# Performance work log

Measured on AMD Instinct MI355X. Metric: run time of the kernel, lower is better.

Reference implementation:

```python
import jax, jax.numpy as jnp
import numpy as np

EPS = 1e-5      # BatchNorm1d default eps
K = 4           # branching factor of the ontology tree
HID = 6         # num_hiddens_genotype
LEVEL_SIZES = (64, 16, 4, 1)   # leaves -> root (term_layer_list order)
OFFSETS = (0, 64, 80, 84)      # slices into the stacked [85,...] term params


def setup_inputs() -> dict:
    key = jax.random.key(0)
    ks = jax.random.split(key, 8)
    B, G, GD, NT, NL = 4096, 4096, 24, 85, 64
    f32 = jnp.float32
    return {
        "x": jax.random.normal(ks[0], (B, G), f32),
        "gene_W": jax.random.normal(ks[1], (NL, GD, G), f32) * (1.0 / np.sqrt(G)),
        "gene_b": jnp.zeros((NL, GD), f32),
        "term_W": jax.random.normal(ks[2], (NT, HID, GD), f32) * (1.0 / np.sqrt(GD)),
        "term_b": jnp.zeros((NT, HID), f32),
        "bn_gamma": jnp.ones((NT, HID), f32),
        "bn_beta": jnp.zeros((NT, HID), f32),
        "aux1_W": jax.random.normal(ks[3], (NT, 1, HID), f32) * 0.1,
        "aux1_b": jnp.zeros((NT, 1), f32),
        "aux2_W": jax.random.normal(ks[4], (NT, 1, 1), f32) * 0.1,
        "aux2_b": jnp.zeros((NT, 1), f32),
        "final_W": jax.random.normal(ks[5], (HID, HID), f32) * (1.0 / np.sqrt(HID)),
        "final_b": jnp.zeros((HID,), f32),
        "fbn_gamma": jnp.ones((HID,), f32),
        "fbn_beta": jnp.zeros((HID,), f32),
        "faux_W": jax.random.normal(ks[6], (1, HID), f32) * 0.1,
        "faux_b": jnp.zeros((1,), f32),
        "fout_W": jax.random.normal(ks[7], (1, 1), f32) * 0.1,
        "fout_b": jnp.zeros((1,), f32),
    }


def _bn(z, g, b):
    # training-mode BatchNorm1d: batch mean / biased variance over axis 0
    mu = jnp.mean(z, axis=0, keepdims=True)
    var = jnp.mean((z - mu) ** 2, axis=0, keepdims=True)
    return (z - mu) * jax.lax.rsqrt(var + EPS) * g + b


def _forward(x, gene_W, gene_b, term_W, term_b, bn_gamma, bn_beta,
             aux1_W, aux1_b, aux2_W, aux2_b, final_W, final_b,
             fbn_gamma, fbn_beta, faux_W, faux_b, fout_W, fout_b):
    B = x.shape[0]
    # direct_gene_layers for all 64 leaf terms, batched: [B, 64, 24]
    h_in = jnp.einsum('bg,tkg->btk', x, gene_W) + gene_b
    aux_outs = []
    h = None
    for n, o in zip(LEVEL_SIZES, OFFSETS):  # leaves -> root (DAG topo order)
        if h is not None:
            # concat the K=4 children hidden states of each term: [B,n,K*HID]
            h_in = h.reshape(B, n, K * HID)
        # per-term Linear + tanh + BatchNorm, batched over the n terms
        z = jnp.tanh(jnp.einsum('bti,thi->bth', h_in, term_W[o:o + n]) + term_b[o:o + n])
        h = _bn(z, bn_gamma[o:o + n], bn_beta[o:o + n])  # [B, n, HID]
        # aux head: Linear(HID->1) -> tanh -> Linear(1->1)
        a1 = jnp.tanh(jnp.einsum('bth,toh->bto', h, aux1_W[o:o + n]) + aux1_b[o:o + n])
        a2 = a1 * aux2_W[o:o + n, 0] + aux2_b[o:o + n]   # [B, n, 1]
        aux_outs.append(a2[..., 0])
    root = h[:, 0, :]                                    # [B, HID]
    f = jnp.tanh(root @ final_W.T + final_b)
    mu = jnp.mean(f, axis=0)
    var = jnp.mean((f - mu) ** 2, axis=0)
    f = (f - mu) * jax.lax.rsqrt(var + EPS) * fbn_gamma + fbn_beta
    fa = jnp.tanh(f @ faux_W.T + faux_b)                 # [B, 1]
    pred = jax.nn.sigmoid(fa * fout_W[0, 0] + fout_b)    # [B, 1]
    # aux_out_map flattened in topo order, with 'final' prediction last: [B, 86]
    return jnp.concatenate(aux_outs + [pred], axis=1)


def reference(x, gene_W, gene_b, term_W, term_b, bn_gamma, bn_beta,
              aux1_W, aux1_b, aux2_W, aux2_b, final_W, final_b,
              fbn_gamma, fbn_beta, faux_W, faux_b, fout_W, fout_b):
    return _forward(x, gene_W, gene_b, term_W, term_b, bn_gamma, bn_beta,
                    aux1_W, aux1_b, aux2_W, aux2_b, final_W, final_b,
                    fbn_gamma, fbn_beta, faux_W, faux_b, fout_W, fout_b)
```

## Files before the change

kernel.cpp:

```cpp
#include <hip/hip_runtime.h>
#include <stdint.h>
#include <math.h>

#define EPSV   1e-5f
#define BATCH  4096
#define GDIM   4096
#define NF0    384
#define NSPLIT 8

typedef __attribute__((ext_vector_type(8))) short bf16x8;
typedef __attribute__((ext_vector_type(4))) float f32x4;
typedef __attribute__((ext_vector_type(2))) float f32x2;
typedef __attribute__((ext_vector_type(4))) uint32_t u32x4;

__device__ __forceinline__ uint32_t pkbf(float x, float y) {
    uint32_t a = __float_as_uint(x) + 0x8000u;
    uint32_t b = __float_as_uint(y) + 0x8000u;
    return __builtin_amdgcn_perm(b, a, 0x07060302u);
}
__device__ __forceinline__ uint16_t f2bf(float f) {
    return (uint16_t)((__float_as_uint(f) + 0x8000u) >> 16);
}
__device__ __forceinline__ float blo(uint32_t v) {
    union { uint32_t u; float f; } x; x.u = v << 16; return x.f;
}
__device__ __forceinline__ float bhi(uint32_t v) {
    union { uint32_t u; float f; } x; x.u = v & 0xffff0000u; return x.f;
}
__device__ __forceinline__ void glds16(const uint16_t* g, short* l) {
    __builtin_amdgcn_global_load_lds(
        (const __attribute__((address_space(1))) void*)g,
        (__attribute__((address_space(3))) void*)l, 16, 0, 0);
}

__global__ __launch_bounds__(256) void prep_kernel(
    const float* __restrict__ gene_W,
    const float* __restrict__ term_W, const float* __restrict__ term_b,
    const float* __restrict__ gene_b,
    uint16_t* __restrict__ m0, float* __restrict__ stats)
{
    const int tid = threadIdx.x;
    if (blockIdx.x == 0) {
        for (int j = tid; j < 1040; j += 256) stats[j] = 0.f;
        for (int f = tid; f < NF0; f += 256) {
            const int t = f / 6, h = f - t * 6;
            float b = term_b[f];
#pragma unroll
            for (int i = 0; i < 24; ++i)
                b += term_W[t * 144 + h * 24 + i] * gene_b[t * 24 + i];
            stats[1040 + f] = b;
        }
    }
    __shared__ float Wl[144];
    const int bid = blockIdx.x;
    const int t = bid >> 4;
    const int g = ((bid & 15) << 8) + tid;
    if (tid < 144) Wl[tid] = term_W[t * 144 + tid];
    __syncthreads();
    float gw[24];
#pragma unroll
    for (int i = 0; i < 24; ++i)
        gw[i] = gene_W[((size_t)t * 24 + i) * GDIM + g];
#pragma unroll
    for (int h = 0; h < 6; ++h) {
        float s = 0.f;
#pragma unroll
        for (int i = 0; i < 24; ++i) s += Wl[h * 24 + i] * gw[i];
        m0[((size_t)(t * 6 + h)) * GDIM + g] = f2bf(s);
    }
}

__global__ __launch_bounds__(256) void gemm_glds(
    const float* __restrict__ A32, const uint16_t* __restrict__ Bw,
    uint16_t* __restrict__ P, int KC)
{
    const int N = NF0, K = GDIM;
    __shared__ short sA[128 * 32];
    __shared__ short sB[2][128 * 32];
    const int tid  = threadIdx.x;
    const int m0   = blockIdx.y * 128, n0 = blockIdx.x * 128;
    const int kbase = blockIdx.z * KC;
    uint16_t* Cp = P + (size_t)blockIdx.z * ((size_t)BATCH * NF0);
    const int wave = tid >> 6, lane = tid & 63;
    const int wm   = (wave & 1) << 6, wn = (wave >> 1) << 6;
    const int lm   = lane & 15, quad = lane >> 4;

    f32x4 acc[4][4];
#pragma unroll
    for (int i = 0; i < 4; ++i)
#pragma unroll
        for (int j = 0; j < 4; ++j) acc[i][j] = (f32x4){0.f, 0.f, 0.f, 0.f};

    const int r0  = tid >> 2;
    const int c0e = (tid & 3) << 3;
    const float*    gA = A32 + (size_t)(m0 + r0) * K + kbase + c0e;
    const uint16_t* gB = Bw  + (size_t)(n0 + r0) * K + kbase + c0e;
    short* la0 = &sA[tid * 8];
    short* la1 = &sA[2048 + tid * 8];
    const size_t rowskip = (size_t)64 * K;

    glds16(gB,            &sB[0][tid * 8]);
    glds16(gB + rowskip,  &sB[0][2048 + tid * 8]);
    f32x4 a0 = *(const f32x4*)(gA);
    f32x4 a1 = *(const f32x4*)(gA + 4);
    f32x4 a2 = *(const f32x4*)(gA + rowskip);
    f32x4 a3 = *(const f32x4*)(gA + rowskip + 4);

    int cur = 0;
    for (int k0 = 0; k0 < KC - 32; k0 += 32) {
        const int kn = k0 + 32;
        glds16(gB + kn,           &sB[cur ^ 1][tid * 8]);
        glds16(gB + rowskip + kn, &sB[cur ^ 1][2048 + tid * 8]);
        f32x4 n0v = *(const f32x4*)(gA + kn);
        f32x4 n1v = *(const f32x4*)(gA + kn + 4);
        f32x4 n2v = *(const f32x4*)(gA + rowskip + kn);
        f32x4 n3v = *(const f32x4*)(gA + rowskip + kn + 4);
        asm volatile("s_waitcnt vmcnt(6)" ::: "memory");
        u32x4 pa0 = (u32x4){pkbf(a0[0],a0[1]), pkbf(a0[2],a0[3]),
                            pkbf(a1[0],a1[1]), pkbf(a1[2],a1[3])};
        u32x4 pa1 = (u32x4){pkbf(a2[0],a2[1]), pkbf(a2[2],a2[3]),
                            pkbf(a3[0],a3[1]), pkbf(a3[2],a3[3])};
        *(u32x4*)la0 = pa0;
        *(u32x4*)la1 = pa1;
        asm volatile("s_waitcnt lgkmcnt(0)" ::: "memory");
        __builtin_amdgcn_s_barrier();
        bf16x8 af[4], bfr[4];
#pragma unroll
        for (int m = 0; m < 4; ++m)
            af[m]  = *(const bf16x8*)&sA[(wm + m * 16 + lm) * 32 + quad * 8];
#pragma unroll
        for (int n = 0; n < 4; ++n)
            bfr[n] = *(const bf16x8*)&sB[cur][(wn + n * 16 + lm) * 32 + quad * 8];
#pragma unroll
        for (int m = 0; m < 4; ++m)
#pragma unroll
            for (int n = 0; n < 4; ++n)
                acc[m][n] = __builtin_amdgcn_mfma_f32_16x16x32_bf16(
                    af[m], bfr[n], acc[m][n], 0, 0, 0);
        __builtin_amdgcn_s_barrier();
        a0 = n0v; a1 = n1v; a2 = n2v; a3 = n3v;
        cur ^= 1;
    }
    asm volatile("s_waitcnt vmcnt(0)" ::: "memory");
    {
        u32x4 pa0 = (u32x4){pkbf(a0[0],a0[1]), pkbf(a0[2],a0[3]),
                            pkbf(a1[0],a1[1]), pkbf(a1[2],a1[3])};
        u32x4 pa1 = (u32x4){pkbf(a2[0],a2[1]), pkbf(a2[2],a2[3]),
                            pkbf(a3[0],a3[1]), pkbf(a3[2],a3[3])};
        *(u32x4*)la0 = pa0;
        *(u32x4*)la1 = pa1;
    }
    asm volatile("s_waitcnt lgkmcnt(0)" ::: "memory");
    __builtin_amdgcn_s_barrier();
    {
        bf16x8 af[4], bfr[4];
#pragma unroll
        for (int m = 0; m < 4; ++m)
            af[m]  = *(const bf16x8*)&sA[(wm + m * 16 + lm) * 32 + quad * 8];
#pragma unroll
        for (int n = 0; n < 4; ++n)
            bfr[n] = *(const bf16x8*)&sB[cur][(wn + n * 16 + lm) * 32 + quad * 8];
#pragma unroll
        for (int m = 0; m < 4; ++m)
#pragma unroll
            for (int n = 0; n < 4; ++n)
                acc[m][n] = __builtin_amdgcn_mfma_f32_16x16x32_bf16(
                    af[m], bfr[n], acc[m][n], 0, 0, 0);
    }
#pragma unroll
    for (int n = 0; n < 4; ++n) {
        const int col = n0 + wn + n * 16 + lm;
#pragma unroll
        for (int m = 0; m < 4; ++m) {
            const int row = m0 + wm + m * 16 + (quad << 2);
            uint16_t* cp = Cp + (size_t)row * N + col;
#pragma unroll
            for (int r = 0; r < 4; ++r) cp[(size_t)r * N] = f2bf(acc[m][n][r]);
        }
    }
}

__global__ __launch_bounds__(256) void lzero_kernel(
    const uint16_t* __restrict__ P, const float* __restrict__ bias0,
    float* __restrict__ z0, float* __restrict__ st0)
{
    __shared__ float red[4 * 768];
    const int tid  = threadIdx.x;
    const int lane = tid & 63, wave = tid >> 6;
    const uint32_t* P32 = (const uint32_t*)P;

    const f32x2 b0 = ((const f32x2*)bias0)[lane];
    const f32x2 b1 = ((const f32x2*)(bias0 + 128))[lane];
    const f32x2 b2 = ((const f32x2*)(bias0 + 256))[lane];

    float s[6], q[6];
#pragma unroll
    for (int k = 0; k < 6; ++k) { s[k] = 0.f; q[k] = 0.f; }

    const int rbase = blockIdx.x * 8 + wave * 2;
    for (int rl = 0; rl < 2; ++rl) {
        const int r = rbase + rl;
        float a0 = b0[0], a1 = b0[1], a2 = b1[0], a3 = b1[1], a4 = b2[0], a5 = b2[1];
        const uint32_t* pr = P32 + (size_t)r * 192 + lane;
#pragma unroll
        for (int z = 0; z < NSPLIT; ++z) {
            const uint32_t* p = pr + (size_t)z * ((size_t)BATCH * 192);
            uint32_t u0 = p[0], u1 = p[64], u2 = p[128];
            a0 += blo(u0); a1 += bhi(u0);
            a2 += blo(u1); a3 += bhi(u1);
            a4 += blo(u2); a5 += bhi(u2);
        }
        float z0v = tanhf(a0), z1v = tanhf(a1), z2v = tanhf(a2);
        float z3v = tanhf(a3), z4v = tanhf(a4), z5v = tanhf(a5);
        f32x2* zr = (f32x2*)(z0 + (size_t)r * NF0);
        zr[lane]       = (f32x2){z0v, z1v};
        zr[64 + lane]  = (f32x2){z2v, z3v};
        zr[128 + lane] = (f32x2){z4v, z5v};
        s[0] += z0v; q[0] += z0v * z0v;
        s[1] += z1v; q[1] += z1v * z1v;
        s[2] += z2v; q[2] += z2v * z2v;
        s[3] += z3v; q[3] += z3v * z3v;
        s[4] += z4v; q[4] += z4v * z4v;
        s[5] += z5v; q[5] += z5v * z5v;
    }
    float* rw = &red[wave * 768 + lane * 12];
#pragma unroll
    for (int k = 0; k < 6; ++k) { rw[k] = s[k]; rw[6 + k] = q[k]; }
    __syncthreads();
    for (int idx = tid; idx < 768; idx += 256) {
        float v = red[idx] + red[768 + idx] + red[1536 + idx] + red[2304 + idx];
        const int l = idx / 12, k = idx - l * 12;
        const int k6 = k % 6;
        const int f = (k6 >> 1) * 128 + 2 * l + (k6 & 1);
        atomicAdd(&st0[(k >= 6 ? NF0 : 0) + f], v);
    }
}

template <int N, int ROWS, int OFF, int PREV_OFF>
__global__ __launch_bounds__(256) void level_kernel(
    const float* __restrict__ in, float* __restrict__ z_out,
    const float* __restrict__ stats_prev, float* __restrict__ stats_out,
    const float* __restrict__ term_W, const float* __restrict__ term_b,
    const float* __restrict__ bn_gamma, const float* __restrict__ bn_beta,
    const float* __restrict__ aux1_W, const float* __restrict__ aux1_b,
    const float* __restrict__ aux2_W, const float* __restrict__ aux2_b,
    float* __restrict__ out)
{
    constexpr int IN_W  = 24 * N;
    constexpr int NFv   = 6 * N;
    constexpr int NG    = 256 / N;
    constexpr int ITERS = (ROWS * N) / 256;
    constexpr int NPREV = 4 * N;

    __shared__ float Wl[144 * N];
    __shared__ float tbl[6 * N];
    __shared__ float aA[IN_W];
    __shared__ float aC[IN_W];
    __shared__ float a1wL[6 * NPREV];
    __shared__ float a1bL[NPREV], a2wL[NPREV], a2bL[NPREV];
    __shared__ float ps[NG * NFv], pq[NG * NFv];

    const int tid = threadIdx.x;
    for (int idx = tid; idx < 144 * N; idx += 256) {
        int t = idx / 144, fh = idx - t * 144;
        Wl[fh * N + t] = term_W[(OFF + t) * 144 + fh];
    }
    for (int idx = tid; idx < 6 * N; idx += 256) {
        int t = idx / 6, h = idx - t * 6;
        tbl[h * N + t] = term_b[(OFF + t) * 6 + h];
    }
    {
        const float invB = 1.0f / BATCH;
        for (int j = tid; j < IN_W; j += 256) {
            float s = stats_prev[j], q = stats_prev[IN_W + j];
            float mu = s * invB;
            float var = q * invB - mu * mu;
            float rstd = rsqrtf(var + EPSV);
            float a = rstd * bn_gamma[PREV_OFF * 6 + j];
            int t = j / 24, i = j - t * 24;
            aA[i * N + t] = a;
            aC[i * N + t] = bn_beta[PREV_OFF * 6 + j] - mu * a;
        }
        for (int idx = tid; idx < 6 * NPREV; idx += 256) {
            int t = idx / 6, h = idx - t * 6;
            a1wL[h * NPREV + t] = aux1_W[(PREV_OFF + t) * 6 + h];
        }
        for (int t = tid; t < NPREV; t += 256) {
            a1bL[t] = aux1_b[PREV_OFF + t];
            a2wL[t] = aux2_W[PREV_OFF + t];
            a2bL[t] = aux2_b[PREV_OFF + t];
        }
    }
    __syncthreads();

    const int term = tid & (N - 1);
    const int grp  = tid / N;
    float s6[6], q6[6];
#pragma unroll
    for (int h = 0; h < 6; ++h) { s6[h] = 0.f; q6[h] = 0.f; }

    for (int it = 0; it < ITERS; ++it) {
        const int r = blockIdx.x * ROWS + it * NG + grp;
        const float* inrow = in + (size_t)r * IN_W + term * 24;
        float hv[24];
#pragma unroll
        for (int i4 = 0; i4 < 6; ++i4) {
            f32x4 v = *(const f32x4*)(inrow + 4 * i4);
            hv[4*i4+0] = v[0]; hv[4*i4+1] = v[1];
            hv[4*i4+2] = v[2]; hv[4*i4+3] = v[3];
        }
#pragma unroll
        for (int i = 0; i < 24; ++i)
            hv[i] = hv[i] * aA[i * N + term] + aC[i * N + term];
#pragma unroll
        for (int s = 0; s < 4; ++s) {
            const int tp = term * 4 + s;
            float acc = a1bL[tp];
#pragma unroll
            for (int h2 = 0; h2 < 6; ++h2) acc += hv[s * 6 + h2] * a1wL[h2 * NPREV + tp];
            float a1 = tanhf(acc);
            out[(size_t)r * 86 + PREV_OFF + tp] = a1 * a2wL[tp] + a2bL[tp];
        }
        float za[6];
#pragma unroll
        for (int h = 0; h < 6; ++h) za[h] = tbl[h * N + term];
#pragma unroll
        for (int i = 0; i < 24; ++i) {
            const float x = hv[i];
#pragma unroll
            for (int h = 0; h < 6; ++h) za[h] += x * Wl[(h * 24 + i) * N + term];
        }
        float* zr = z_out + (size_t)r * NFv + term * 6;
#pragma unroll
        for (int h = 0; h < 6; ++h) {
            float z = tanhf(za[h]);
            zr[h] = z;
            s6[h] += z;
            q6[h] += z * z;
        }
    }
#pragma unroll
    for (int h = 0; h < 6; ++h) {
        ps[grp * NFv + term * 6 + h] = s6[h];
        pq[grp * NFv + term * 6 + h] = q6[h];
    }
    __syncthreads();
    for (int f = tid; f < NFv; f += 256) {
        float s = 0.f, q = 0.f;
        for (int g2 = 0; g2 < NG; ++g2) { s += ps[g2 * NFv + f]; q += pq[g2 * NFv + f]; }
        atomicAdd(&stats_out[f], s);
        atomicAdd(&stats_out[NFv + f], q);
    }
}

__global__ __launch_bounds__(256) void final_p1(
    const float* __restrict__ z3, const float* __restrict__ st3,
    const float* __restrict__ bn_gamma, const float* __restrict__ bn_beta,
    const float* __restrict__ aux1_W, const float* __restrict__ aux1_b,
    const float* __restrict__ aux2_W, const float* __restrict__ aux2_b,
    const float* __restrict__ final_W, const float* __restrict__ final_b,
    float* __restrict__ fbuf, float* __restrict__ stf,
    float* __restrict__ out)
{
    __shared__ float wred[4][12];
    const int tid = threadIdx.x;
    const int r = blockIdx.x * 256 + tid;
    const float invB = 1.0f / BATCH;
    float a[6], c[6];
#pragma unroll
    for (int j = 0; j < 6; ++j) {
        float s = st3[j], q = st3[6 + j];
        float mu = s * invB, var = q * invB - mu * mu;
        float rstd = rsqrtf(var + EPSV);
        a[j] = rstd * bn_gamma[504 + j];
        c[j] = bn_beta[504 + j] - mu * a[j];
    }
    float h[6];
    {
        f32x2 z01 = *(const f32x2*)(z3 + (size_t)r * 6);
        f32x2 z23 = *(const f32x2*)(z3 + (size_t)r * 6 + 2);
        f32x2 z45 = *(const f32x2*)(z3 + (size_t)r * 6 + 4);
        h[0] = z01[0] * a[0] + c[0]; h[1] = z01[1] * a[1] + c[1];
        h[2] = z23[0] * a[2] + c[2]; h[3] = z23[1] * a[3] + c[3];
        h[4] = z45[0] * a[4] + c[4]; h[5] = z45[1] * a[5] + c[5];
    }
    float acc = aux1_b[84];
#pragma unroll
    for (int j = 0; j < 6; ++j) acc += h[j] * aux1_W[504 + j];
    out[(size_t)r * 86 + 84] = tanhf(acc) * aux2_W[84] + aux2_b[84];

    float f[6], s6[6], q6[6];
#pragma unroll
    for (int j = 0; j < 6; ++j) {
        float s = final_b[j];
#pragma unroll
        for (int k = 0; k < 6; ++k) s += h[k] * final_W[j * 6 + k];
        f[j] = tanhf(s);
        s6[j] = f[j]; q6[j] = f[j] * f[j];
    }
    {
        f32x2* fr = (f32x2*)(fbuf + (size_t)r * 6);
        fr[0] = (f32x2){f[0], f[1]};
        fr[1] = (f32x2){f[2], f[3]};
        fr[2] = (f32x2){f[4], f[5]};
    }
#pragma unroll
    for (int off = 32; off >= 1; off >>= 1) {
#pragma unroll
        for (int j = 0; j < 6; ++j) {
            s6[j] += __shfl_xor(s6[j], off, 64);
            q6[j] += __shfl_xor(q6[j], off, 64);
        }
    }
    const int wv = tid >> 6, ln = tid & 63;
    if (ln == 0) {
#pragma unroll
        for (int j = 0; j < 6; ++j) { wred[wv][j] = s6[j]; wred[wv][6 + j] = q6[j]; }
    }
    __syncthreads();
    if (tid < 12) {
        float s = wred[0][tid] + wred[1][tid] + wred[2][tid] + wred[3][tid];
        atomicAdd(&stf[tid], s);
    }
}

__global__ __launch_bounds__(256) void final_p2(
    const float* __restrict__ fbuf, const float* __restrict__ stf,
    const float* __restrict__ fbn_gamma, const float* __restrict__ fbn_beta,
    const float* __restrict__ faux_W, const float* __restrict__ faux_b,
    const float* __restrict__ fout_W, const float* __restrict__ fout_b,
    float* __restrict__ out)
{
    const int tid = threadIdx.x;
    const int r = blockIdx.x * 256 + tid;
    const float invB = 1.0f / BATCH;
    float av[6], cv[6];
#pragma unroll
    for (int j = 0; j < 6; ++j) {
        float mu = stf[j] * invB, var = stf[6 + j] * invB - mu * mu;
        float rstd = rsqrtf(var + EPSV);
        av[j] = rstd * fbn_gamma[j];
        cv[j] = fbn_beta[j] - mu * av[j];
    }
    float f[6];
    {
        f32x2 f01 = *(const f32x2*)(fbuf + (size_t)r * 6);
        f32x2 f23 = *(const f32x2*)(fbuf + (size_t)r * 6 + 2);
        f32x2 f45 = *(const f32x2*)(fbuf + (size_t)r * 6 + 4);
        f[0] = f01[0]; f[1] = f01[1]; f[2] = f23[0];
        f[3] = f23[1]; f[4] = f45[0]; f[5] = f45[1];
    }
    float acc2 = faux_b[0];
#pragma unroll
    for (int j = 0; j < 6; ++j) acc2 += (f[j] * av[j] + cv[j]) * faux_W[j];
    float fa  = tanhf(acc2);
    float pre = fa * fout_W[0] + fout_b[0];
    out[(size_t)r * 86 + 85] = 1.0f / (1.0f + expf(-pre));
}

extern "C" void kernel_launch(void* const* d_in, const int* in_sizes, int n_in,
                              void* d_out, int out_size, void* d_ws, size_t ws_size,
                              hipStream_t stream)
{
    const float* x      = (const float*)d_in[0];
    const float* gene_W = (const float*)d_in[1];
    const float* gene_b = (const float*)d_in[2];
    const float* term_W = (const float*)d_in[3];
    const float* term_b = (const float*)d_in[4];
    const float* bn_g   = (const float*)d_in[5];
    const float* bn_b   = (const float*)d_in[6];
    const float* a1W    = (const float*)d_in[7];
    const float* a1b    = (const float*)d_in[8];
    const float* a2W    = (const float*)d_in[9];
    const float* a2b    = (const float*)d_in[10];
    const float* fW     = (const float*)d_in[11];
    const float* fb     = (const float*)d_in[12];
    const float* fbn_g  = (const float*)d_in[13];
    const float* fbn_b  = (const float*)d_in[14];
    const float* fxW    = (const float*)d_in[15];
    const float* fxb    = (const float*)d_in[16];
    const float* foW    = (const float*)d_in[17];
    const float* fob    = (const float*)d_in[18];
    float* out = (float*)d_out;

    const size_t M0B = (size_t)NF0 * GDIM * 2;
    const size_t PB  = (size_t)NSPLIT * BATCH * NF0 * 2;
    const size_t Z0B = (size_t)BATCH * NF0 * 4;

    char* ws = (char*)d_ws;
    uint16_t* m0b  = (uint16_t*)ws;
    uint16_t* pbuf = (uint16_t*)(ws + M0B);
    float*    z0   = (float*)(ws + M0B + PB);
    float*    z1   = (float*)(ws + M0B + PB + Z0B);
    float*    z2   = (float*)(ws + M0B + PB + Z0B + 1572864);
    float*    z3   = (float*)(ws + M0B + PB + Z0B + 1572864 + 393216);
    float*    stats = (float*)(ws + M0B + PB + Z0B + 1572864 + 393216 + 98304);
    float* st0 = stats;
    float* st1 = stats + 768;
    float* st2 = stats + 960;
    float* st3 = stats + 1008;
    float* stf = stats + 1020;
    float* bias0 = stats + 1040;
    float* fbuf  = stats + 2048;

    prep_kernel<<<1024, 256, 0, stream>>>(gene_W, term_W, term_b, gene_b,
                                          m0b, stats);
    gemm_glds<<<dim3(3, 32, NSPLIT), 256, 0, stream>>>(x, m0b, pbuf, GDIM / NSPLIT);
    lzero_kernel<<<512, 256, 0, stream>>>(pbuf, bias0, z0, st0);
    level_kernel<16, 16, 64, 0><<<256, 256, 0, stream>>>(
        z0, z1, st0, st1, term_W, term_b, bn_g, bn_b, a1W, a1b, a2W, a2b, out);
    level_kernel<4, 64, 80, 64><<<64, 256, 0, stream>>>(
        z1, z2, st1, st2, term_W, term_b, bn_g, bn_b, a1W, a1b, a2W, a2b, out);
    level_kernel<1, 256, 84, 80><<<16, 256, 0, stream>>>(
        z2, z3, st2, st3, term_W, term_b, bn_g, bn_b, a1W, a1b, a2W, a2b, out);
    final_p1<<<16, 256, 0, stream>>>(
        z3, st3, bn_g, bn_b, a1W, a1b, a2W, a2b, fW, fb, fbuf, stf, out);
    final_p2<<<16, 256, 0, stream>>>(
        fbuf, stf, fbn_g, fbn_b, fxW, fxb, foW, fob, out);
}
```

Baseline: 244.5 us.

## Widen GEMM tile to full N with 512-thread blocks to read x once

Each GEMM block now computes a 128x384 output tile covering the whole N dimension, using 8 waves each owning a 64x96 sub-tile. Previously three blocks per row tile each loaded and converted the fp32 x tile. The change removes that redundant global read and the repeated bf16 packing. In exchange it raises LDS use and accumulator registers per wave, and the grid drops to 256 blocks, which lowers occupancy and latency hiding.

```diff
diff --git a/kernel.cpp b/kernel.cpp
--- a/kernel.cpp
+++ b/kernel.cpp
@@ -70,106 +70,98 @@
     }
 }
 
-__global__ __launch_bounds__(256) void gemm_glds(
+__global__ __launch_bounds__(512) void gemm_wide(
     const float* __restrict__ A32, const uint16_t* __restrict__ Bw,
     uint16_t* __restrict__ P, int KC)
 {
     const int N = NF0, K = GDIM;
     __shared__ short sA[128 * 32];
-    __shared__ short sB[2][128 * 32];
+    __shared__ short sB[2][384 * 32];
     const int tid  = threadIdx.x;
-    const int m0   = blockIdx.y * 128, n0 = blockIdx.x * 128;
-    const int kbase = blockIdx.z * KC;
-    uint16_t* Cp = P + (size_t)blockIdx.z * ((size_t)BATCH * NF0);
+    const int m0   = blockIdx.x * 128;
+    const int kbase = blockIdx.y * KC;
+    uint16_t* Cp = P + (size_t)blockIdx.y * ((size_t)BATCH * NF0);
     const int wave = tid >> 6, lane = tid & 63;
-    const int wm   = (wave & 1) << 6, wn = (wave >> 1) << 6;
+    const int wm   = (wave >> 2) * 64;
+    const int wn   = (wave & 3) * 96;
     const int lm   = lane & 15, quad = lane >> 4;
 
-    f32x4 acc[4][4];
+    f32x4 acc[4][6];
 #pragma unroll
     for (int i = 0; i < 4; ++i)
 #pragma unroll
-        for (int j = 0; j < 4; ++j) acc[i][j] = (f32x4){0.f, 0.f, 0.f, 0.f};
+        for (int j = 0; j < 6; ++j) acc[i][j] = (f32x4){0.f, 0.f, 0.f, 0.f};
 
     const int r0  = tid >> 2;
     const int c0e = (tid & 3) << 3;
     const float*    gA = A32 + (size_t)(m0 + r0) * K + kbase + c0e;
-    const uint16_t* gB = Bw  + (size_t)(n0 + r0) * K + kbase + c0e;
-    short* la0 = &sA[tid * 8];
-    short* la1 = &sA[2048 + tid * 8];
-    const size_t rowskip = (size_t)64 * K;
-
-    glds16(gB,            &sB[0][tid * 8]);
-    glds16(gB + rowskip,  &sB[0][2048 + tid * 8]);
+    const uint16_t* gB = Bw  + (size_t)r0 * K + kbase + c0e;
+    const size_t bskip = (size_t)128 * K;
+    short* la = &sA[tid * 8];
+
+    glds16(gB,             &sB[0][tid * 8]);
+    glds16(gB + bskip,     &sB[0][4096 + tid * 8]);
+    glds16(gB + 2 * bskip, &sB[0][8192 + tid * 8]);
     f32x4 a0 = *(const f32x4*)(gA);
     f32x4 a1 = *(const f32x4*)(gA + 4);
-    f32x4 a2 = *(const f32x4*)(gA + rowskip);
-    f32x4 a3 = *(const f32x4*)(gA + rowskip + 4);
 
     int cur = 0;
     for (int k0 = 0; k0 < KC - 32; k0 += 32) {
         const int kn = k0 + 32;
-        glds16(gB + kn,           &sB[cur ^ 1][tid * 8]);
-        glds16(gB + rowskip + kn, &sB[cur ^ 1][2048 + tid * 8]);
+        glds16(gB + kn,             &sB[cur ^ 1][tid * 8]);
+        glds16(gB + bskip + kn,     &sB[cur ^ 1][4096 + tid * 8]);
+        glds16(gB + 2 * bskip + kn, &sB[cur ^ 1][8192 + tid * 8]);
         f32x4 n0v = *(const f32x4*)(gA + kn);
         f32x4 n1v = *(const f32x4*)(gA + kn + 4);
-        f32x4 n2v = *(const f32x4*)(gA + rowskip + kn);
-        f32x4 n3v = *(const f32x4*)(gA + rowskip + kn + 4);
-        asm volatile("s_waitcnt vmcnt(6)" ::: "memory");
-        u32x4 pa0 = (u32x4){pkbf(a0[0],a0[1]), pkbf(a0[2],a0[3]),
-                            pkbf(a1[0],a1[1]), pkbf(a1[2],a1[3])};
-        u32x4 pa1 = (u32x4){pkbf(a2[0],a2[1]), pkbf(a2[2],a2[3]),
-                            pkbf(a3[0],a3[1]), pkbf(a3[2],a3[3])};
-        *(u32x4*)la0 = pa0;
-        *(u32x4*)la1 = pa1;
+        asm volatile("s_waitcnt vmcnt(5)" ::: "memory");
+        u32x4 pa = (u32x4){pkbf(a0[0],a0[1]), pkbf(a0[2],a0[3]),
+                           pkbf(a1[0],a1[1]), pkbf(a1[2],a1[3])};
+        *(u32x4*)la = pa;
         asm volatile("s_waitcnt lgkmcnt(0)" ::: "memory");
         __builtin_amdgcn_s_barrier();
-        bf16x8 af[4], bfr[4];
+        bf16x8 af[4], bfr[6];
 #pragma unroll
         for (int m = 0; m < 4; ++m)
             af[m]  = *(const bf16x8*)&sA[(wm + m * 16 + lm) * 32 + quad * 8];
 #pragma unroll
-        for (int n = 0; n < 4; ++n)
+        for (int n = 0; n < 6; ++n)
             bfr[n] = *(const bf16x8*)&sB[cur][(wn + n * 16 + lm) * 32 + quad * 8];
 #pragma unroll
         for (int m = 0; m < 4; ++m)
 #pragma unroll
-            for (int n = 0; n < 4; ++n)
+            for (int n = 0; n < 6; ++n)
                 acc[m][n] = __builtin_amdgcn_mfma_f32_16x16x32_bf16(
                     af[m], bfr[n], acc[m][n], 0, 0, 0);
         __builtin_amdgcn_s_barrier();
-        a0 = n0v; a1 = n1v; a2 = n2v; a3 = n3v;
+        a0 = n0v; a1 = n1v;
         cur ^= 1;
     }
     asm volatile("s_waitcnt vmcnt(0)" ::: "memory");
     {
-        u32x4 pa0 = (u32x4){pkbf(a0[0],a0[1]), pkbf(a0[2],a0[3]),
-                            pkbf(a1[0],a1[1]), pkbf(a1[2],a1[3])};
-        u32x4 pa1 = (u32x4){pkbf(a2[0],a2[1]), pkbf(a2[2],a2[3]),
-                            pkbf(a3[0],a3[1]), pkbf(a3[2],a3[3])};
-        *(u32x4*)la0 = pa0;
-        *(u32x4*)la1 = pa1;
+        u32x4 pa = (u32x4){pkbf(a0[0],a0[1]), pkbf(a0[2],a0[3]),
+                           pkbf(a1[0],a1[1]), pkbf(a1[2],a1[3])};
+        *(u32x4*)la = pa;
     }
     asm volatile("s_waitcnt lgkmcnt(0)" ::: "memory");
     __builtin_amdgcn_s_barrier();
     {
-        bf16x8 af[4], bfr[4];
+        bf16x8 af[4], bfr[6];
 #pragma unroll
         for (int m = 0; m < 4; ++m)
             af[m]  = *(const bf16x8*)&sA[(wm + m * 16 + lm) * 32 + quad * 8];
 #pragma unroll
-        for (int n = 0; n < 4; ++n)
+        for (int n = 0; n < 6; ++n)
             bfr[n] = *(const bf16x8*)&sB[cur][(wn + n * 16 + lm) * 32 + quad * 8];
 #pragma unroll
         for (int m = 0; m < 4; ++m)
 #pragma unroll
-            for (int n = 0; n < 4; ++n)
+            for (int n = 0; n < 6; ++n)
                 acc[m][n] = __builtin_amdgcn_mfma_f32_16x16x32_bf16(
                     af[m], bfr[n], acc[m][n], 0, 0, 0);
     }
 #pragma unroll
-    for (int n = 0; n < 4; ++n) {
-        const int col = n0 + wn + n * 16 + lm;
+    for (int n = 0; n < 6; ++n) {
+        const int col = wn + n * 16 + lm;
 #pragma unroll
         for (int m = 0; m < 4; ++m) {
             const int row = m0 + wm + m * 16 + (quad << 2);
@@ -505,7 +497,7 @@
 
     prep_kernel<<<1024, 256, 0, stream>>>(gene_W, term_W, term_b, gene_b,
                                           m0b, stats);
-    gemm_glds<<<dim3(3, 32, NSPLIT), 256, 0, stream>>>(x, m0b, pbuf, GDIM / NSPLIT);
+    gemm_wide<<<dim3(32, NSPLIT), 512, 0, stream>>>(x, m0b, pbuf, GDIM / NSPLIT);
     lzero_kernel<<<512, 256, 0, stream>>>(pbuf, bias0, z0, st0);
     level_kernel<16, 16, 64, 0><<<256, 256, 0, stream>>>(
         z0, z1, st0, st1, term_W, term_b, bn_g, bn_b, a1W, a1b, a2W, a2b, out);
```

Result: no change. 240.6 us (-1.6%).
